# Optimization experiments

Measured on AMD Instinct MI355X. Metric: run time of the kernel, lower is better.

## Reference

```python
import jax, jax.numpy as jnp
import numpy as np

B, T = 64, 2048
DEC, ENC, ATT, LOC, K = 1024, 512, 128, 32, 31


def setup_inputs() -> dict:
    key = jax.random.key(0)
    ks = jax.random.split(key, 9)
    inv = lambda n: 1.0 / np.sqrt(n)
    return {
        "query": jax.random.normal(ks[0], (B, DEC), dtype=jnp.float32),
        "values": jax.random.normal(ks[1], (B, T, ENC), dtype=jnp.float32),
        "cumulative_attention_weights": jax.random.uniform(ks[2], (B, T), dtype=jnp.float32),
        "mask": jnp.zeros((B, T), dtype=bool),
        "Q_w": jax.random.uniform(ks[3], (ATT, DEC), jnp.float32, -inv(DEC), inv(DEC)),
        "Q_b": jax.random.uniform(ks[4], (ATT,), jnp.float32, -inv(DEC), inv(DEC)),
        "V_w": jax.random.uniform(ks[5], (ATT, ENC), jnp.float32, -inv(ENC), inv(ENC)),
        "conv_w": jax.random.uniform(ks[6], (LOC, 1, K), jnp.float32, -inv(K), inv(K)),
        "loc_proj_w": jax.random.uniform(ks[7], (ATT, LOC), jnp.float32, -inv(LOC), inv(LOC)),
        "v_w": jax.random.uniform(ks[8], (1, ATT), jnp.float32, -inv(ATT), inv(ATT)),
    }


def reference(query, values, cumulative_attention_weights, mask,
              Q_w, Q_b, V_w, conv_w, loc_proj_w, v_w):
    # query projection: [B, 1, ATT] (broadcast over T)
    q = query @ Q_w.T + Q_b                       # [B, ATT]
    q = q[:, None, :]
    # values cache: [B, T, ATT]
    v_cache = jnp.einsum("bte,ae->bta", values, V_w)
    # location features: Conv1d(1 -> LOC, k=31, same padding) over cum weights
    x = cumulative_attention_weights[:, None, :]   # [B, 1, T]
    loc = jax.lax.conv_general_dilated(
        x, conv_w, window_strides=(1,), padding="SAME",
        dimension_numbers=("NCH", "OIH", "NCH"))   # [B, LOC, T]
    loc = jnp.einsum("bct,ac->bta", loc, loc_proj_w)  # [B, T, ATT]
    # additive attention energies
    energies = jnp.tanh(q + v_cache + loc) @ v_w[0]   # [B, T]
    energies = jnp.where(mask, -jnp.inf, energies)
    attention_weights = jax.nn.softmax(energies, axis=1)
    # context: [B, ENC]
    attention_context = jnp.einsum("bt,bte->be", attention_weights, values)
    return attention_context, attention_weights
```

## Files before the change

kernel.cpp:

```cpp
#include <hip/hip_runtime.h>
#include <hip/hip_bf16.h>
#include <math.h>

#define B_  64
#define T_  2048
#define DEC_ 1024
#define ENC_ 512
#define ATT_ 128
#define LOC_ 32
#define KW_  31

typedef __attribute__((ext_vector_type(8))) short short8;
typedef __attribute__((ext_vector_type(4))) float f32x4;

__device__ inline unsigned short bf16_rn(float x) {
    unsigned int u = __builtin_bit_cast(unsigned int, x);
    unsigned int r = u + 0x7fffu + ((u >> 16) & 1u);
    return (unsigned short)(r >> 16);
}
__device__ inline float bf16_to_f(unsigned short h) {
    unsigned int u = ((unsigned int)h) << 16;
    return __builtin_bit_cast(float, u);
}

__global__ __launch_bounds__(256) void prep_kernel(
    const float* __restrict__ query, const float* __restrict__ Q_w,
    const float* __restrict__ Q_b, const float* __restrict__ conv_w,
    const float* __restrict__ loc_proj_w, const float* __restrict__ V_w,
    float* __restrict__ qbuf,
    unsigned short* __restrict__ Bhi, unsigned short* __restrict__ Blo,
    unsigned short* __restrict__ effThi, unsigned short* __restrict__ effTlo)
{
    int bi = blockIdx.x, tid = threadIdx.x;
    if (bi < B_) {
        __shared__ float sq[DEC_];
        *(float4*)(&sq[tid * 4]) = *(const float4*)(query + bi * DEC_ + tid * 4);
        __syncthreads();
        int w = tid >> 6, lane = tid & 63;
        for (int a = w * 32; a < w * 32 + 32; ++a) {
            const float* row = Q_w + (size_t)a * DEC_;
            float s = 0.f;
            #pragma unroll
            for (int i = 0; i < 4; ++i) {
                float4 qw = *(const float4*)(row + i * 256 + lane * 4);
                float4 xq = *(const float4*)(sq + i * 256 + lane * 4);
                s += qw.x * xq.x + qw.y * xq.y + qw.z * xq.z + qw.w * xq.w;
            }
            #pragma unroll
            for (int m = 32; m >= 1; m >>= 1) s += __shfl_xor(s, m, 64);
            if (lane == 0) qbuf[bi * ATT_ + a] = s + Q_b[a];
        }
    } else if (bi == B_) {
        if (tid < ATT_) {
            int n = tid;
            for (int k = 0; k < 32; ++k) {
                float s = 0.f;
                if (k < KW_)
                    for (int c = 0; c < LOC_; ++c)
                        s += loc_proj_w[n * LOC_ + c] * conv_w[c * KW_ + k];
                unsigned short h = bf16_rn(s);
                float lo = s - bf16_to_f(h);
                effThi[n * 32 + k] = h;
                effTlo[n * 32 + k] = bf16_rn(lo);
            }
        }
    } else {
        int g0 = (bi - B_ - 1) * 512;
        #pragma unroll
        for (int p = 0; p < 2; ++p) {
            int gi = g0 + p * 256 + tid;
            float4 v = ((const float4*)V_w)[gi];
            ushort4 h4, l4;
            h4.x = bf16_rn(v.x); l4.x = bf16_rn(v.x - bf16_to_f(h4.x));
            h4.y = bf16_rn(v.y); l4.y = bf16_rn(v.y - bf16_to_f(h4.y));
            h4.z = bf16_rn(v.z); l4.z = bf16_rn(v.z - bf16_to_f(h4.z));
            h4.w = bf16_rn(v.w); l4.w = bf16_rn(v.w - bf16_to_f(h4.w));
            *(ushort4*)(Bhi + (size_t)gi * 4) = h4;
            *(ushort4*)(Blo + (size_t)gi * 4) = l4;
        }
    }
}

#define KC 64
#define LDA 72

__global__ __launch_bounds__(256) void energy_kernel(
    const float* __restrict__ values, const float* __restrict__ cum,
    const float* __restrict__ qbuf,
    const unsigned short* __restrict__ Bhi, const unsigned short* __restrict__ Blo,
    const unsigned short* __restrict__ effThi, const unsigned short* __restrict__ effTlo,
    const float* __restrict__ vw, float* __restrict__ energies)
{
    __shared__ unsigned short sAh[128 * LDA];
    __shared__ unsigned short sAl[128 * LDA];
    __shared__ unsigned short sBh[128 * LDA];
    __shared__ unsigned short sBl[128 * LDA];
    __shared__ float sx[160];
    __shared__ float sred[256];

    const int tid = threadIdx.x;
    const int bx  = blockIdx.x;
    const int b   = bx >> 4;
    const int t0  = (bx & 15) * 128;

    if (tid < 128 + 2 * 15) {
        int g = t0 - 15 + tid;
        sx[tid] = (g >= 0 && g < T_) ? cum[b * T_ + g] : 0.f;
    }

    const int w      = tid >> 6;
    const int lane   = tid & 63;
    const int lane15 = lane & 15;
    const int quad   = lane >> 4;
    const int wm0    = (w & 1) * 64;
    const int wn0    = (w >> 1) * 64;

    f32x4 acc[4][4];
    #pragma unroll
    for (int i = 0; i < 4; ++i)
        #pragma unroll
        for (int j = 0; j < 4; ++j) acc[i][j] = (f32x4){0.f, 0.f, 0.f, 0.f};

    const float* aptr = values + ((size_t)b * T_ + t0) * ENC_;

    for (int kc = 0; kc < ENC_; kc += KC) {
        __syncthreads();
        #pragma unroll
        for (int p = 0; p < 8; ++p) {
            int fi = p * 256 + tid;
            int r = fi >> 4, c4 = (fi & 15) * 4;
            float4 v = *(const float4*)(aptr + (size_t)r * ENC_ + kc + c4);
            ushort4 h4, l4;
            h4.x = bf16_rn(v.x); l4.x = bf16_rn(v.x - bf16_to_f(h4.x));
            h4.y = bf16_rn(v.y); l4.y = bf16_rn(v.y - bf16_to_f(h4.y));
            h4.z = bf16_rn(v.z); l4.z = bf16_rn(v.z - bf16_to_f(h4.z));
            h4.w = bf16_rn(v.w); l4.w = bf16_rn(v.w - bf16_to_f(h4.w));
            *(ushort4*)(&sAh[r * LDA + c4]) = h4;
            *(ushort4*)(&sAl[r * LDA + c4]) = l4;
        }
        {
            int n = tid >> 1, koff = (tid & 1) * 32;
            const unsigned short* srch = Bhi + (size_t)n * ENC_ + kc + koff;
            const unsigned short* srcl = Blo + (size_t)n * ENC_ + kc + koff;
            #pragma unroll
            for (int q4 = 0; q4 < 4; ++q4) {
                *(uint4*)(&sBh[n * LDA + koff + q4 * 8]) = *(const uint4*)(srch + q4 * 8);
                *(uint4*)(&sBl[n * LDA + koff + q4 * 8]) = *(const uint4*)(srcl + q4 * 8);
            }
        }
        __syncthreads();

        #pragma unroll
        for (int ks = 0; ks < KC; ks += 32) {
            const int base = ks + quad * 8;
            short8 ah[4], al[4], bh[4], bl[4];
            #pragma unroll
            for (int i = 0; i < 4; ++i) {
                int row = (wm0 + i * 16 + lane15) * LDA + base;
                ah[i] = *(const short8*)(&sAh[row]);
                al[i] = *(const short8*)(&sAl[row]);
            }
            #pragma unroll
            for (int j = 0; j < 4; ++j) {
                int row = (wn0 + j * 16 + lane15) * LDA + base;
                bh[j] = *(const short8*)(&sBh[row]);
                bl[j] = *(const short8*)(&sBl[row]);
            }
            #pragma unroll
            for (int i = 0; i < 4; ++i)
                #pragma unroll
                for (int j = 0; j < 4; ++j) {
                    acc[i][j] = __builtin_amdgcn_mfma_f32_16x16x32_bf16(ah[i], bh[j], acc[i][j], 0, 0, 0);
                    acc[i][j] = __builtin_amdgcn_mfma_f32_16x16x32_bf16(ah[i], bl[j], acc[i][j], 0, 0, 0);
                    acc[i][j] = __builtin_amdgcn_mfma_f32_16x16x32_bf16(al[i], bh[j], acc[i][j], 0, 0, 0);
                }
        }
    }

    __syncthreads();
    #pragma unroll
    for (int p = 0; p < 16; ++p) {
        int idx = p * 256 + tid;
        int r = idx >> 5, k = idx & 31;
        float xv = (k < KW_) ? sx[r + k] : 0.f;
        unsigned short h = bf16_rn(xv);
        sAh[r * LDA + k] = h;
        sAl[r * LDA + k] = bf16_rn(xv - bf16_to_f(h));
        sBh[r * LDA + k] = effThi[idx];
        sBl[r * LDA + k] = effTlo[idx];
    }
    __syncthreads();
    {
        const int base = quad * 8;
        short8 ah[4], al[4], bh[4], bl[4];
        #pragma unroll
        for (int i = 0; i < 4; ++i) {
            int row = (wm0 + i * 16 + lane15) * LDA + base;
            ah[i] = *(const short8*)(&sAh[row]);
            al[i] = *(const short8*)(&sAl[row]);
        }
        #pragma unroll
        for (int j = 0; j < 4; ++j) {
            int row = (wn0 + j * 16 + lane15) * LDA + base;
            bh[j] = *(const short8*)(&sBh[row]);
            bl[j] = *(const short8*)(&sBl[row]);
        }
        #pragma unroll
        for (int i = 0; i < 4; ++i)
            #pragma unroll
            for (int j = 0; j < 4; ++j) {
                acc[i][j] = __builtin_amdgcn_mfma_f32_16x16x32_bf16(ah[i], bh[j], acc[i][j], 0, 0, 0);
                acc[i][j] = __builtin_amdgcn_mfma_f32_16x16x32_bf16(ah[i], bl[j], acc[i][j], 0, 0, 0);
                acc[i][j] = __builtin_amdgcn_mfma_f32_16x16x32_bf16(al[i], bh[j], acc[i][j], 0, 0, 0);
            }
    }

    float qv[4], vv[4];
    #pragma unroll
    for (int j = 0; j < 4; ++j) {
        int n = wn0 + j * 16 + lane15;
        qv[j] = qbuf[b * ATT_ + n];
        vv[j] = vw[n];
    }
    #pragma unroll
    for (int i = 0; i < 4; ++i) {
        #pragma unroll
        for (int reg = 0; reg < 4; ++reg) {
            float s = 0.f;
            #pragma unroll
            for (int j = 0; j < 4; ++j) {
                float z = acc[i][j][reg] + qv[j];
                s += vv[j] * tanhf(z);
            }
            #pragma unroll
            for (int m = 8; m >= 1; m >>= 1) s += __shfl_xor(s, m, 64);
            if (lane15 == 0)
                sred[(w >> 1) * 128 + wm0 + i * 16 + quad * 4 + reg] = s;
        }
    }
    __syncthreads();
    if (tid < 128)
        energies[b * T_ + t0 + tid] = sred[tid] + sred[128 + tid];
}

__global__ __launch_bounds__(256) void softmax_kernel(
    const float* __restrict__ energies, const unsigned char* __restrict__ mask,
    float* __restrict__ out)
{
    int b = blockIdx.x, tid = threadIdx.x;
    float* ctx  = out;
    float* wout = out + B_ * ENC_;

    for (int i = tid; i < ENC_; i += 256) ctx[b * ENC_ + i] = 0.f;

    float e[8];
    float mx = -INFINITY;
    #pragma unroll
    for (int p = 0; p < 8; ++p) {
        int t = p * 256 + tid;
        float v = energies[b * T_ + t];
        if (mask[b * T_ + t]) v = -INFINITY;
        e[p] = v;
        mx = fmaxf(mx, v);
    }
    #pragma unroll
    for (int m = 32; m >= 1; m >>= 1) mx = fmaxf(mx, __shfl_xor(mx, m, 64));
    __shared__ float red[8];
    int wave = tid >> 6;
    if ((tid & 63) == 0) red[wave] = mx;
    __syncthreads();
    mx = fmaxf(fmaxf(red[0], red[1]), fmaxf(red[2], red[3]));

    float sum = 0.f;
    #pragma unroll
    for (int p = 0; p < 8; ++p) {
        e[p] = expf(e[p] - mx);
        sum += e[p];
    }
    #pragma unroll
    for (int m = 32; m >= 1; m >>= 1) sum += __shfl_xor(sum, m, 64);
    if ((tid & 63) == 0) red[4 + wave] = sum;
    __syncthreads();
    sum = red[4] + red[5] + red[6] + red[7];
    float inv = 1.f / sum;
    #pragma unroll
    for (int p = 0; p < 8; ++p)
        wout[b * T_ + p * 256 + tid] = e[p] * inv;
}

__global__ __launch_bounds__(256) void context_kernel(
    const float* __restrict__ values, const float* __restrict__ w,
    float* __restrict__ ctx)
{
    int bs = blockIdx.x;
    int b = bs >> 3, seg = bs & 7;
    int tid = threadIdx.x;
    int tt = tid >> 7;
    int e4 = (tid & 127) * 4;

    __shared__ float sw[256];
    int tbase = seg * 256;
    sw[tid] = w[b * T_ + tbase + tid];
    __syncthreads();

    float4 acc = make_float4(0.f, 0.f, 0.f, 0.f);
    const float* vp = values + ((size_t)b * T_ + tbase) * ENC_ + e4;
    #pragma unroll 4
    for (int t = tt; t < 256; t += 2) {
        float4 v = *(const float4*)(vp + (size_t)t * ENC_);
        float wv = sw[t];
        acc.x += wv * v.x; acc.y += wv * v.y;
        acc.z += wv * v.z; acc.w += wv * v.w;
    }

    __shared__ float red[512];
    if (tt == 1) *(float4*)&red[e4] = acc;
    __syncthreads();
    if (tt == 0) {
        float4 o = *(const float4*)&red[e4];
        atomicAdd(&ctx[b * ENC_ + e4 + 0], acc.x + o.x);
        atomicAdd(&ctx[b * ENC_ + e4 + 1], acc.y + o.y);
        atomicAdd(&ctx[b * ENC_ + e4 + 2], acc.z + o.z);
        atomicAdd(&ctx[b * ENC_ + e4 + 3], acc.w + o.w);
    }
}

extern "C" void kernel_launch(void* const* d_in, const int* in_sizes, int n_in,
                              void* d_out, int out_size, void* d_ws, size_t ws_size,
                              hipStream_t stream) {
    const float* query        = (const float*)d_in[0];
    const float* values       = (const float*)d_in[1];
    const float* cum          = (const float*)d_in[2];
    const unsigned char* mask = (const unsigned char*)d_in[3];
    const float* Q_w          = (const float*)d_in[4];
    const float* Q_b          = (const float*)d_in[5];
    const float* V_w          = (const float*)d_in[6];
    const float* conv_w       = (const float*)d_in[7];
    const float* loc_proj_w   = (const float*)d_in[8];
    const float* v_w          = (const float*)d_in[9];

    float* out = (float*)d_out;
    char*  ws  = (char*)d_ws;
    float*          qbuf     = (float*)(ws);
    float*          energies = (float*)(ws + 32768);
    unsigned short* Bhi      = (unsigned short*)(ws + 557056);
    unsigned short* Blo      = (unsigned short*)(ws + 688128);
    unsigned short* effThi   = (unsigned short*)(ws + 819200);
    unsigned short* effTlo   = (unsigned short*)(ws + 827392);

    prep_kernel<<<97, 256, 0, stream>>>(query, Q_w, Q_b, conv_w, loc_proj_w, V_w,
                                        qbuf, Bhi, Blo, effThi, effTlo);
    energy_kernel<<<1024, 256, 0, stream>>>(values, cum, qbuf, Bhi, Blo,
                                            effThi, effTlo, v_w, energies);
    softmax_kernel<<<B_, 256, 0, stream>>>(energies, mask, out);
    context_kernel<<<B_ * 8, 256, 0, stream>>>(values, out + B_ * ENC_, out);
}
```

Baseline: 524.5 us.

## Stream V_w fragments from global, prefetch values tiles, reshape context grid

V_w hi/lo is repacked in the prep kernel into a 32-wide chunked layout, so the energy kernel loads B fragments straight from global/L2 instead of staging them in LDS. This halves LDS use, and launch_bounds now requests 3 blocks per CU. The values tile for the next K chunk is prefetched into registers while MFMAs run on the current one. The context kernel uses 16 segments per batch with contiguous per-half T ranges, and the prep kernel gets small tweaks (two rows per iteration, weights staged in shared memory). Risks are register pressure from the prefetch buffers and repeated global reads of B fragments by every block.

```diff
diff --git a/kernel.cpp b/kernel.cpp
--- a/kernel.cpp
+++ b/kernel.cpp
@@ -28,8 +28,8 @@
     const float* __restrict__ Q_b, const float* __restrict__ conv_w,
     const float* __restrict__ loc_proj_w, const float* __restrict__ V_w,
     float* __restrict__ qbuf,
-    unsigned short* __restrict__ Bhi, unsigned short* __restrict__ Blo,
-    unsigned short* __restrict__ effThi, unsigned short* __restrict__ effTlo)
+    unsigned short* __restrict__ Bph, unsigned short* __restrict__ Bpl,
+    unsigned short* __restrict__ effh, unsigned short* __restrict__ effl)
 {
     int bi = blockIdx.x, tid = threadIdx.x;
     if (bi < B_) {
@@ -37,31 +37,45 @@
         *(float4*)(&sq[tid * 4]) = *(const float4*)(query + bi * DEC_ + tid * 4);
         __syncthreads();
         int w = tid >> 6, lane = tid & 63;
-        for (int a = w * 32; a < w * 32 + 32; ++a) {
-            const float* row = Q_w + (size_t)a * DEC_;
-            float s = 0.f;
+        for (int a = w * 32; a < w * 32 + 32; a += 2) {
+            const float* r0 = Q_w + (size_t)a * DEC_;
+            const float* r1 = r0 + DEC_;
+            float s0 = 0.f, s1 = 0.f;
             #pragma unroll
             for (int i = 0; i < 4; ++i) {
-                float4 qw = *(const float4*)(row + i * 256 + lane * 4);
+                float4 q0 = *(const float4*)(r0 + i * 256 + lane * 4);
+                float4 q1 = *(const float4*)(r1 + i * 256 + lane * 4);
                 float4 xq = *(const float4*)(sq + i * 256 + lane * 4);
-                s += qw.x * xq.x + qw.y * xq.y + qw.z * xq.z + qw.w * xq.w;
-            }
-            #pragma unroll
-            for (int m = 32; m >= 1; m >>= 1) s += __shfl_xor(s, m, 64);
-            if (lane == 0) qbuf[bi * ATT_ + a] = s + Q_b[a];
+                s0 += q0.x * xq.x + q0.y * xq.y + q0.z * xq.z + q0.w * xq.w;
+                s1 += q1.x * xq.x + q1.y * xq.y + q1.z * xq.z + q1.w * xq.w;
+            }
+            #pragma unroll
+            for (int m = 32; m >= 1; m >>= 1) {
+                s0 += __shfl_xor(s0, m, 64);
+                s1 += __shfl_xor(s1, m, 64);
+            }
+            if (lane == 0) {
+                qbuf[bi * ATT_ + a]     = s0 + Q_b[a];
+                qbuf[bi * ATT_ + a + 1] = s1 + Q_b[a + 1];
+            }
         }
     } else if (bi == B_) {
+        __shared__ float slp[ATT_ * LOC_];
+        __shared__ float scw[LOC_ * KW_];
+        for (int i = tid; i < ATT_ * LOC_; i += 256) slp[i] = loc_proj_w[i];
+        for (int i = tid; i < LOC_ * KW_; i += 256) scw[i] = conv_w[i];
+        __syncthreads();
         if (tid < ATT_) {
             int n = tid;
             for (int k = 0; k < 32; ++k) {
                 float s = 0.f;
                 if (k < KW_)
+                    #pragma unroll
                     for (int c = 0; c < LOC_; ++c)
-                        s += loc_proj_w[n * LOC_ + c] * conv_w[c * KW_ + k];
+                        s += slp[n * LOC_ + c] * scw[c * KW_ + k];
                 unsigned short h = bf16_rn(s);
-                float lo = s - bf16_to_f(h);
-                effThi[n * 32 + k] = h;
-                effTlo[n * 32 + k] = bf16_rn(lo);
+                effh[n * 32 + k] = h;
+                effl[n * 32 + k] = bf16_rn(s - bf16_to_f(h));
             }
         }
     } else {
@@ -69,14 +83,17 @@
         #pragma unroll
         for (int p = 0; p < 2; ++p) {
             int gi = g0 + p * 256 + tid;
+            int n  = gi >> 7;
+            int kq = (gi & 127) * 4;
             float4 v = ((const float4*)V_w)[gi];
             ushort4 h4, l4;
             h4.x = bf16_rn(v.x); l4.x = bf16_rn(v.x - bf16_to_f(h4.x));
             h4.y = bf16_rn(v.y); l4.y = bf16_rn(v.y - bf16_to_f(h4.y));
             h4.z = bf16_rn(v.z); l4.z = bf16_rn(v.z - bf16_to_f(h4.z));
             h4.w = bf16_rn(v.w); l4.w = bf16_rn(v.w - bf16_to_f(h4.w));
-            *(ushort4*)(Bhi + (size_t)gi * 4) = h4;
-            *(ushort4*)(Blo + (size_t)gi * 4) = l4;
+            int dst = (kq >> 5) * 4096 + n * 32 + (kq & 31);
+            *(ushort4*)(Bph + dst) = h4;
+            *(ushort4*)(Bpl + dst) = l4;
         }
     }
 }
@@ -84,17 +101,15 @@
 #define KC 64
 #define LDA 72
 
-__global__ __launch_bounds__(256) void energy_kernel(
+__global__ __launch_bounds__(256, 3) void energy_kernel(
     const float* __restrict__ values, const float* __restrict__ cum,
     const float* __restrict__ qbuf,
-    const unsigned short* __restrict__ Bhi, const unsigned short* __restrict__ Blo,
-    const unsigned short* __restrict__ effThi, const unsigned short* __restrict__ effTlo,
+    const unsigned short* __restrict__ Bph, const unsigned short* __restrict__ Bpl,
+    const unsigned short* __restrict__ effh, const unsigned short* __restrict__ effl,
     const float* __restrict__ vw, float* __restrict__ energies)
 {
     __shared__ unsigned short sAh[128 * LDA];
     __shared__ unsigned short sAl[128 * LDA];
-    __shared__ unsigned short sBh[128 * LDA];
-    __shared__ unsigned short sBl[128 * LDA];
     __shared__ float sx[160];
     __shared__ float sred[256];
 
@@ -103,7 +118,7 @@
     const int b   = bx >> 4;
     const int t0  = (bx & 15) * 128;
 
-    if (tid < 128 + 2 * 15) {
+    if (tid < 158) {
         int g = t0 - 15 + tid;
         sx[tid] = (g >= 0 && g < T_) ? cum[b * T_ + g] : 0.f;
     }
@@ -122,38 +137,39 @@
         for (int j = 0; j < 4; ++j) acc[i][j] = (f32x4){0.f, 0.f, 0.f, 0.f};
 
     const float* aptr = values + ((size_t)b * T_ + t0) * ENC_;
+    const int ar = tid >> 4;
+    const int ac = (tid & 15) * 4;
+
+    float4 pf[8];
+    #pragma unroll
+    for (int p = 0; p < 8; ++p)
+        pf[p] = *(const float4*)(aptr + (size_t)(p * 16 + ar) * ENC_ + ac);
 
     for (int kc = 0; kc < ENC_; kc += KC) {
         __syncthreads();
         #pragma unroll
         for (int p = 0; p < 8; ++p) {
-            int fi = p * 256 + tid;
-            int r = fi >> 4, c4 = (fi & 15) * 4;
-            float4 v = *(const float4*)(aptr + (size_t)r * ENC_ + kc + c4);
+            int r = p * 16 + ar;
+            float4 v = pf[p];
             ushort4 h4, l4;
             h4.x = bf16_rn(v.x); l4.x = bf16_rn(v.x - bf16_to_f(h4.x));
             h4.y = bf16_rn(v.y); l4.y = bf16_rn(v.y - bf16_to_f(h4.y));
             h4.z = bf16_rn(v.z); l4.z = bf16_rn(v.z - bf16_to_f(h4.z));
             h4.w = bf16_rn(v.w); l4.w = bf16_rn(v.w - bf16_to_f(h4.w));
-            *(ushort4*)(&sAh[r * LDA + c4]) = h4;
-            *(ushort4*)(&sAl[r * LDA + c4]) = l4;
-        }
-        {
-            int n = tid >> 1, koff = (tid & 1) * 32;
-            const unsigned short* srch = Bhi + (size_t)n * ENC_ + kc + koff;
-            const unsigned short* srcl = Blo + (size_t)n * ENC_ + kc + koff;
-            #pragma unroll
-            for (int q4 = 0; q4 < 4; ++q4) {
-                *(uint4*)(&sBh[n * LDA + koff + q4 * 8]) = *(const uint4*)(srch + q4 * 8);
-                *(uint4*)(&sBl[n * LDA + koff + q4 * 8]) = *(const uint4*)(srcl + q4 * 8);
-            }
+            *(ushort4*)(&sAh[r * LDA + ac]) = h4;
+            *(ushort4*)(&sAl[r * LDA + ac]) = l4;
         }
         __syncthreads();
-
+        if (kc + KC < ENC_) {
+            #pragma unroll
+            for (int p = 0; p < 8; ++p)
+                pf[p] = *(const float4*)(aptr + (size_t)(p * 16 + ar) * ENC_ + kc + KC + ac);
+        }
         #pragma unroll
         for (int ks = 0; ks < KC; ks += 32) {
-            const int base = ks + quad * 8;
-            short8 ah[4], al[4], bh[4], bl[4];
+            const int base  = ks + quad * 8;
+            const int chunk = ((kc + ks) >> 5) * 4096;
+            short8 ah[4], al[4];
             #pragma unroll
             for (int i = 0; i < 4; ++i) {
                 int row = (wm0 + i * 16 + lane15) * LDA + base;
@@ -162,18 +178,16 @@
             }
             #pragma unroll
             for (int j = 0; j < 4; ++j) {
-                int row = (wn0 + j * 16 + lane15) * LDA + base;
-                bh[j] = *(const short8*)(&sBh[row]);
-                bl[j] = *(const short8*)(&sBl[row]);
-            }
-            #pragma unroll
-            for (int i = 0; i < 4; ++i)
+                int n = wn0 + j * 16 + lane15;
+                short8 bh = *(const short8*)(Bph + chunk + n * 32 + quad * 8);
+                short8 bl = *(const short8*)(Bpl + chunk + n * 32 + quad * 8);
                 #pragma unroll
-                for (int j = 0; j < 4; ++j) {
-                    acc[i][j] = __builtin_amdgcn_mfma_f32_16x16x32_bf16(ah[i], bh[j], acc[i][j], 0, 0, 0);
-                    acc[i][j] = __builtin_amdgcn_mfma_f32_16x16x32_bf16(ah[i], bl[j], acc[i][j], 0, 0, 0);
-                    acc[i][j] = __builtin_amdgcn_mfma_f32_16x16x32_bf16(al[i], bh[j], acc[i][j], 0, 0, 0);
+                for (int i = 0; i < 4; ++i) {
+                    acc[i][j] = __builtin_amdgcn_mfma_f32_16x16x32_bf16(ah[i], bh, acc[i][j], 0, 0, 0);
+                    acc[i][j] = __builtin_amdgcn_mfma_f32_16x16x32_bf16(ah[i], bl, acc[i][j], 0, 0, 0);
+                    acc[i][j] = __builtin_amdgcn_mfma_f32_16x16x32_bf16(al[i], bh, acc[i][j], 0, 0, 0);
                 }
+            }
         }
     }
 
@@ -186,13 +200,11 @@
         unsigned short h = bf16_rn(xv);
         sAh[r * LDA + k] = h;
         sAl[r * LDA + k] = bf16_rn(xv - bf16_to_f(h));
-        sBh[r * LDA + k] = effThi[idx];
-        sBl[r * LDA + k] = effTlo[idx];
     }
     __syncthreads();
     {
         const int base = quad * 8;
-        short8 ah[4], al[4], bh[4], bl[4];
+        short8 ah[4], al[4];
         #pragma unroll
         for (int i = 0; i < 4; ++i) {
             int row = (wm0 + i * 16 + lane15) * LDA + base;
@@ -201,18 +213,16 @@
         }
         #pragma unroll
         for (int j = 0; j < 4; ++j) {
-            int row = (wn0 + j * 16 + lane15) * LDA + base;
-            bh[j] = *(const short8*)(&sBh[row]);
-            bl[j] = *(const short8*)(&sBl[row]);
-        }
-        #pragma unroll
-        for (int i = 0; i < 4; ++i)
-            #pragma unroll
-            for (int j = 0; j < 4; ++j) {
-                acc[i][j] = __builtin_amdgcn_mfma_f32_16x16x32_bf16(ah[i], bh[j], acc[i][j], 0, 0, 0);
-                acc[i][j] = __builtin_amdgcn_mfma_f32_16x16x32_bf16(ah[i], bl[j], acc[i][j], 0, 0, 0);
-                acc[i][j] = __builtin_amdgcn_mfma_f32_16x16x32_bf16(al[i], bh[j], acc[i][j], 0, 0, 0);
-            }
+            int n = wn0 + j * 16 + lane15;
+            short8 bh = *(const short8*)(effh + n * 32 + base);
+            short8 bl = *(const short8*)(effl + n * 32 + base);
+            #pragma unroll
+            for (int i = 0; i < 4; ++i) {
+                acc[i][j] = __builtin_amdgcn_mfma_f32_16x16x32_bf16(ah[i], bh, acc[i][j], 0, 0, 0);
+                acc[i][j] = __builtin_amdgcn_mfma_f32_16x16x32_bf16(ah[i], bl, acc[i][j], 0, 0, 0);
+                acc[i][j] = __builtin_amdgcn_mfma_f32_16x16x32_bf16(al[i], bh, acc[i][j], 0, 0, 0);
+            }
+        }
     }
 
     float qv[4], vv[4];
@@ -292,23 +302,23 @@
     const float* __restrict__ values, const float* __restrict__ w,
     float* __restrict__ ctx)
 {
-    int bs = blockIdx.x;
-    int b = bs >> 3, seg = bs & 7;
+    int bx = blockIdx.x;
+    int b = bx >> 4, seg = bx & 15;
     int tid = threadIdx.x;
     int tt = tid >> 7;
     int e4 = (tid & 127) * 4;
 
-    __shared__ float sw[256];
-    int tbase = seg * 256;
-    sw[tid] = w[b * T_ + tbase + tid];
-    __syncthreads();
-
+    __shared__ float sw[128];
+    if (tid < 128) sw[tid] = w[b * T_ + seg * 128 + tid];
+    __syncthreads();
+
+    const float* vp = values + ((size_t)b * T_ + seg * 128) * ENC_ + e4;
     float4 acc = make_float4(0.f, 0.f, 0.f, 0.f);
-    const float* vp = values + ((size_t)b * T_ + tbase) * ENC_ + e4;
-    #pragma unroll 4
-    for (int t = tt; t < 256; t += 2) {
-        float4 v = *(const float4*)(vp + (size_t)t * ENC_);
-        float wv = sw[t];
+    #pragma unroll 8
+    for (int t = 0; t < 64; ++t) {
+        int tg = tt * 64 + t;
+        float4 v = *(const float4*)(vp + (size_t)tg * ENC_);
+        float wv = sw[tg];
         acc.x += wv * v.x; acc.y += wv * v.y;
         acc.z += wv * v.z; acc.w += wv * v.w;
     }
@@ -343,15 +353,15 @@
     char*  ws  = (char*)d_ws;
     float*          qbuf     = (float*)(ws);
     float*          energies = (float*)(ws + 32768);
-    unsigned short* Bhi      = (unsigned short*)(ws + 557056);
-    unsigned short* Blo      = (unsigned short*)(ws + 688128);
-    unsigned short* effThi   = (unsigned short*)(ws + 819200);
-    unsigned short* effTlo   = (unsigned short*)(ws + 827392);
+    unsigned short* Bph      = (unsigned short*)(ws + 557056);
+    unsigned short* Bpl      = (unsigned short*)(ws + 688128);
+    unsigned short* effh     = (unsigned short*)(ws + 819200);
+    unsigned short* effl     = (unsigned short*)(ws + 827392);
 
     prep_kernel<<<97, 256, 0, stream>>>(query, Q_w, Q_b, conv_w, loc_proj_w, V_w,
-                                        qbuf, Bhi, Blo, effThi, effTlo);
-    energy_kernel<<<1024, 256, 0, stream>>>(values, cum, qbuf, Bhi, Blo,
-                                            effThi, effTlo, v_w, energies);
+                                        qbuf, Bph, Bpl, effh, effl);
+    energy_kernel<<<1024, 256, 0, stream>>>(values, cum, qbuf, Bph, Bpl,
+                                            effh, effl, v_w, energies);
     softmax_kernel<<<B_, 256, 0, stream>>>(energies, mask, out);
-    context_kernel<<<B_ * 8, 256, 0, stream>>>(values, out + B_ * ENC_, out);
-}
+    context_kernel<<<B_ * 16, 256, 0, stream>>>(values, out + B_ * ENC_, out);
+}
```

New measurement: 493.2 us. -6.0%, faster.
